# Performance work log

Hardware: AMD Instinct MI355X
Metric: run time of the kernel (lower is better)

## Reference

```python
import jax, jax.numpy as jnp
import numpy as np

ALPHA = 0.25
GAMMA = 2.0
W_CLASS = W_BBOX = W_GIOU = W_MASK = W_DICE = W_PROJ = 1.0
EPS = 1e-8


def box_cxcywh_to_xyxy(b):
    cx, cy, w, h = jnp.split(b, 4, axis=-1)
    return jnp.concatenate([cx - 0.5 * w, cy - 0.5 * h, cx + 0.5 * w, cy + 0.5 * h], axis=-1)


def dice_coef(inputs, targets):
    # inputs: logits [N, D]; targets: binary [M, D]
    s = jax.nn.sigmoid(inputs)
    num = 2.0 * jnp.einsum('nd,md->nm', s, targets)
    den = s.sum(-1)[:, None] + targets.sum(-1)[None, :]
    return (num + 1.0) / (den + 1.0)  # [N, M]


def sigmoid_focal_coef(inputs, targets):
    # inputs: logits [N, D]; targets: binary [M, D] -> [N, M]
    x = inputs[:, None, :]
    t = targets[None, :, :]
    p = jax.nn.sigmoid(x)
    # BCE-with-logits, numerically stable
    ce = jnp.maximum(x, 0.0) - x * t + jnp.log1p(jnp.exp(-jnp.abs(x)))
    p_t = p * t + (1.0 - p) * (1.0 - t)
    alpha_t = ALPHA * t + (1.0 - ALPHA) * (1.0 - t)
    return (alpha_t * ce * (1.0 - p_t) ** GAMMA).mean(-1)


def giou_cost(src_xyxy, tgt_xyxy):
    # src [nf, nq, 4], tgt [nf, 1, 4] -> cost [nf, nq, 1]
    a1 = (src_xyxy[..., 2] - src_xyxy[..., 0]) * (src_xyxy[..., 3] - src_xyxy[..., 1])
    a2 = (tgt_xyxy[..., 2] - tgt_xyxy[..., 0]) * (tgt_xyxy[..., 3] - tgt_xyxy[..., 1])
    lt = jnp.maximum(src_xyxy[:, :, None, :2], tgt_xyxy[:, None, :, :2])
    rb = jnp.minimum(src_xyxy[:, :, None, 2:], tgt_xyxy[:, None, :, 2:])
    wh = jnp.clip(rb - lt, 0.0)
    inter = wh[..., 0] * wh[..., 1]
    union = a1[:, :, None] + a2[:, None, :] - inter
    iou = inter / union
    ltc = jnp.minimum(src_xyxy[:, :, None, :2], tgt_xyxy[:, None, :, :2])
    rbc = jnp.maximum(src_xyxy[:, :, None, 2:], tgt_xyxy[:, None, :, 2:])
    whc = jnp.clip(rbc - ltc, 0.0)
    areac = whc[..., 0] * whc[..., 1]
    giou = iou - (areac - union) / areac
    return -giou


def cost_matrix_one(logits, boxes, masks, tmask, tbox, tvalid):
    # logits [nf,nq,1], boxes [nf,nq,4], masks [nf,nq,H,W], tmask [nf,H,W], tbox [nf,4], tvalid [nf]
    p = jax.nn.sigmoid(logits[..., 0])  # [nf, nq]
    neg = (1.0 - ALPHA) * p ** GAMMA * (-jnp.log(1.0 - p + EPS))
    pos = ALPHA * (1.0 - p) ** GAMMA * (-jnp.log(p + EPS))
    w = (tvalid != 0).astype(p.dtype)  # valid-frame mask replaces python `continue`
    cost_class = (((pos - neg) * w[:, None]).sum(0) / w.sum())[:, None]  # [nq, 1]

    cost_bbox = jnp.abs(boxes[:, :, None, :] - tbox[:, None, None, :]).sum(-1).mean(0)  # [nq, 1]
    cost_giou = giou_cost(box_cxcywh_to_xyxy(boxes), box_cxcywh_to_xyxy(tbox[:, None, :])).mean(0)

    out_mask = jnp.transpose(masks, (1, 0, 2, 3))  # [nq, nf, H, W]
    nq = out_mask.shape[0]
    flat_src = out_mask.reshape(nq, -1)
    flat_tgt = tmask.reshape(1, -1)
    cost_mask = sigmoid_focal_coef(flat_src, flat_tgt)  # [nq, 1]
    cost_dice = -dice_coef(flat_src, flat_tgt)

    src_y = jnp.max(out_mask, axis=2, keepdims=True).reshape(nq, -1)  # [nq, nf*W]
    src_x = jnp.max(out_mask, axis=3, keepdims=True).reshape(nq, -1)  # [nq, nf*H]
    tgt_y = jnp.max(tmask[None], axis=2, keepdims=True).reshape(1, -1)
    tgt_x = jnp.max(tmask[None], axis=3, keepdims=True).reshape(1, -1)
    cost_proj = -0.5 * (dice_coef(src_y, tgt_y) + dice_coef(src_x, tgt_x))

    C = (W_CLASS * cost_class + W_BBOX * cost_bbox + W_GIOU * cost_giou
         + W_MASK * cost_mask + W_DICE * cost_dice + W_PROJ * cost_proj)
    return C  # [nq, 1]


def setup_inputs() -> dict:
    key = jax.random.key(0)
    k = jax.random.split(key, 6)
    bs, nf, nq, H, W = 2, 8, 300, 96, 96
    pred_logits = jax.random.normal(k[0], (bs, nf, nq, 1), dtype=jnp.float32)
    pred_boxes = jax.random.uniform(k[1], (bs, nf, nq, 4), dtype=jnp.float32)
    pred_masks = jax.random.normal(k[2], (bs, nf, nq, H, W), dtype=jnp.float32)
    target_masks = (jax.random.uniform(k[3], (bs, nf, H, W)) < 0.3).astype(jnp.float32)
    tgt_boxes = jax.random.uniform(k[4], (bs, nf, 4), dtype=jnp.float32)
    tgt_valid = jnp.ones((bs, nf), dtype=jnp.int32)
    valid_pad = jnp.zeros((bs, H, W), dtype=bool)
    return {"pred_logits": pred_logits, "pred_boxes": pred_boxes, "pred_masks": pred_masks,
            "target_masks": target_masks, "tgt_boxes": tgt_boxes, "tgt_valid": tgt_valid,
            "valid_pad": valid_pad}


def reference(pred_logits, pred_boxes, pred_masks, target_masks, tgt_boxes, tgt_valid, valid_pad):
    # zero out predictions over padded regions (masked_fill with valid[:, None, None])
    masks = jnp.where(valid_pad[:, None, None, :, :], 0.0, pred_masks)
    C = jax.vmap(cost_matrix_one)(pred_logits, pred_boxes, masks, target_masks, tgt_boxes, tgt_valid)
    src_ind = jnp.argmin(C, axis=1).astype(jnp.int64)  # [bs, 1]
    tgt_ind = jnp.zeros_like(src_ind)
    return C, src_ind, tgt_ind
```

## Files before the change

### kernel.cpp

```cpp
#include <hip/hip_runtime.h>
#include <math.h>

#define NF 8
#define NQ 300
#define HSZ 96
#define WSZ 96
#define HW (HSZ*WSZ)
#define DTOT (NF*HW)
#define NT 256
#define NBF 16

#define WS_TGTY 0
#define WS_TGTX 1536
#define WS_TSUM 3072
#define WS_YSUM 3088
#define WS_XSUM 3104
#define WS_PART 4096

__device__ __forceinline__ float sigmoid_fast(float x) {
    float e = __expf(-fabsf(x));
    float inv = __builtin_amdgcn_rcpf(1.f + e);
    return x >= 0.f ? inv : e * inv;
}

__device__ __forceinline__ float blockSum(float v, float* red) {
    #pragma unroll
    for (int off = 32; off > 0; off >>= 1) v += __shfl_down(v, off, 64);
    int wid = threadIdx.x >> 6, lane = threadIdx.x & 63;
    __syncthreads();
    if (lane == 0) red[wid] = v;
    __syncthreads();
    return red[0] + red[1] + red[2] + red[3];
}

__global__ __launch_bounds__(NT)
void targets_kernel(const float* __restrict__ tm, float* __restrict__ ws) {
    int bf = blockIdx.x, t = threadIdx.x;
    __shared__ float tile[HSZ * 97];
    __shared__ float red[4];
    const float* base = tm + (size_t)bf * HW;
    float tsum = 0.f;
    #pragma unroll
    for (int it = 0; it < 36; ++it) {
        int e = it * NT + t;
        float v = base[e];
        tsum += v;
        tile[e + e / 96] = v;
    }
    __syncthreads();
    float ysum = 0.f, xsum = 0.f;
    if (t < 96) {
        float m = -INFINITY;
        #pragma unroll 8
        for (int h = 0; h < HSZ; ++h) m = fmaxf(m, tile[h * 97 + t]);
        ws[WS_TGTY + bf * 96 + t] = m;
        ysum = m;
    } else if (t < 192) {
        int hh = t - 96;
        float m = -INFINITY;
        #pragma unroll 8
        for (int w = 0; w < WSZ; ++w) m = fmaxf(m, tile[hh * 97 + w]);
        ws[WS_TGTX + bf * 96 + hh] = m;
        xsum = m;
    }
    tsum = blockSum(tsum, red);
    ysum = blockSum(ysum, red);
    xsum = blockSum(xsum, red);
    if (t == 0) {
        ws[WS_TSUM + bf] = tsum;
        ws[WS_YSUM + bf] = ysum;
        ws[WS_XSUM + bf] = xsum;
    }
}

__global__ __launch_bounds__(NT, 8)
void partial_kernel(const float* __restrict__ masks, const float* __restrict__ tmask,
                    const unsigned char* __restrict__ vpad, const float* __restrict__ ws,
                    float* __restrict__ part) {
    int bf = blockIdx.x / NQ;
    int q  = blockIdx.x - bf * NQ;
    int b  = bf >> 3;
    int t  = threadIdx.x;

    __shared__ unsigned short tile[HSZ * 98];
    __shared__ float red[4];

    const float4* mrow = (const float4*)(masks + (size_t)(bf * NQ + q) * HW);
    const float4* trow = (const float4*)(tmask + (size_t)bf * HW);
    const unsigned* prow = (const unsigned*)(vpad + (size_t)b * HW);

    float focal = 0.f, dnum = 0.f, dden = 0.f;

    #pragma unroll
    for (int it = 0; it < 9; ++it) {
        int i4 = it * NT + t;
        float4 xv = mrow[i4];
        float4 tv = trow[i4];
        unsigned pv = prow[i4];
        int h = i4 / 24;
        int c = (i4 - h * 24) * 4;

        float xs[4] = {xv.x, xv.y, xv.z, xv.w};
        float ts[4] = {tv.x, tv.y, tv.z, tv.w};
        unsigned short us[4];
        #pragma unroll
        for (int j = 0; j < 4; ++j) {
            float x = ((pv >> (8 * j)) & 0xFFu) ? 0.f : xs[j];
            float tg = ts[j];
            float ee = __expf(-fabsf(x));
            float se = 1.f + ee;
            float inv = __builtin_amdgcn_rcpf(se);
            float s = x >= 0.f ? inv : ee * inv;
            float L = __logf(se);
            float ce = fmaxf(x, 0.f) - x * tg + L;
            float omp = s + tg - 2.f * s * tg;
            float at = 0.75f - 0.5f * tg;
            focal = fmaf(at * ce, omp * omp, focal);
            dnum = fmaf(s, tg, dnum);
            dden += s;
            us[j] = (unsigned short)(__float_as_uint(x) >> 16);
        }
        int ta = h * 98 + c;
        *(unsigned*)&tile[ta]     = (unsigned)us[0] | ((unsigned)us[1] << 16);
        *(unsigned*)&tile[ta + 2] = (unsigned)us[2] | ((unsigned)us[3] << 16);
    }
    __syncthreads();

    float pYn = 0.f, pYd = 0.f, pXn = 0.f, pXd = 0.f;
    if (t < 96) {
        float m = -INFINITY;
        #pragma unroll 8
        for (int h = 0; h < HSZ; ++h)
            m = fmaxf(m, __uint_as_float((unsigned)tile[h * 98 + t] << 16));
        float sg = sigmoid_fast(m);
        pYd = sg;
        pYn = sg * ws[WS_TGTY + bf * 96 + t];
    } else if (t < 192) {
        int hh = t - 96;
        float m = -INFINITY;
        #pragma unroll 8
        for (int w = 0; w < WSZ; ++w)
            m = fmaxf(m, __uint_as_float((unsigned)tile[hh * 98 + w] << 16));
        float sg = sigmoid_fast(m);
        pXd = sg;
        pXn = sg * ws[WS_TGTX + bf * 96 + hh];
    }

    focal = blockSum(focal, red);
    dnum  = blockSum(dnum, red);
    dden  = blockSum(dden, red);
    pYn   = blockSum(pYn, red);
    pYd   = blockSum(pYd, red);
    pXn   = blockSum(pXn, red);
    pXd   = blockSum(pXd, red);

    if (t == 0) {
        float* p = part + (size_t)blockIdx.x * 8;
        p[0] = focal; p[1] = dnum; p[2] = dden;
        p[3] = pYn;   p[4] = pYd;  p[5] = pXn;  p[6] = pXd;
    }
}

__global__ __launch_bounds__(NT)
void combine_kernel(const float* __restrict__ logits, const float* __restrict__ boxes,
                    const float* __restrict__ tbox, const int* __restrict__ tvalid,
                    const float* __restrict__ ws, float* __restrict__ out) {
    int gid = blockIdx.x * NT + threadIdx.x;
    if (gid >= 2 * NQ) return;
    int b = gid / NQ, q = gid - b * NQ;

    float focal = 0.f, dnum = 0.f, dden = 0.f;
    float pYn = 0.f, pYd = 0.f, pXn = 0.f, pXd = 0.f;
    float tsum = 0.f, ysum = 0.f, xsum = 0.f;
    #pragma unroll
    for (int f = 0; f < NF; ++f) {
        int bf = b * NF + f;
        const float* p = ws + WS_PART + (size_t)(bf * NQ + q) * 8;
        focal += p[0]; dnum += p[1]; dden += p[2];
        pYn += p[3]; pYd += p[4]; pXn += p[5]; pXd += p[6];
        tsum += ws[WS_TSUM + bf];
        ysum += ws[WS_YSUM + bf];
        xsum += ws[WS_XSUM + bf];
    }
    float cost_mask = focal / (float)DTOT;
    float cost_dice = -(2.f * dnum + 1.f) / (dden + tsum + 1.f);
    float coefY = (2.f * pYn + 1.f) / (pYd + ysum + 1.f);
    float coefX = (2.f * pXn + 1.f) / (pXd + xsum + 1.f);
    float cost_proj = -0.5f * (coefY + coefX);

    float wsum = 0.f, cls = 0.f, cb = 0.f, cg = 0.f;
    #pragma unroll
    for (int f = 0; f < NF; ++f) {
        float wv = (tvalid[b * NF + f] != 0) ? 1.f : 0.f;
        wsum += wv;
        float lg = logits[(b * NF + f) * NQ + q];
        float p = sigmoid_fast(lg);
        float negc = 0.75f * p * p * (-__logf(1.f - p + 1e-8f));
        float posc = 0.25f * (1.f - p) * (1.f - p) * (-__logf(p + 1e-8f));
        cls += (posc - negc) * wv;

        const float* bx = boxes + (size_t)((b * NF + f) * NQ + q) * 4;
        const float* tb = tbox + (b * NF + f) * 4;
        float cx = bx[0], cy = bx[1], bw = bx[2], bh = bx[3];
        float tcx = tb[0], tcy = tb[1], tbw = tb[2], tbh = tb[3];
        cb += fabsf(cx - tcx) + fabsf(cy - tcy) + fabsf(bw - tbw) + fabsf(bh - tbh);
        float sx1 = cx - 0.5f * bw, sy1 = cy - 0.5f * bh;
        float sx2 = cx + 0.5f * bw, sy2 = cy + 0.5f * bh;
        float tx1 = tcx - 0.5f * tbw, ty1 = tcy - 0.5f * tbh;
        float tx2 = tcx + 0.5f * tbw, ty2 = tcy + 0.5f * tbh;
        float a1 = (sx2 - sx1) * (sy2 - sy1), a2 = (tx2 - tx1) * (ty2 - ty1);
        float iw = fmaxf(fminf(sx2, tx2) - fmaxf(sx1, tx1), 0.f);
        float ih = fmaxf(fminf(sy2, ty2) - fmaxf(sy1, ty1), 0.f);
        float inter = iw * ih;
        float uni = a1 + a2 - inter;
        float iou = inter / uni;
        float cw = fmaxf(fmaxf(sx2, tx2) - fminf(sx1, tx1), 0.f);
        float chh = fmaxf(fmaxf(sy2, ty2) - fminf(sy1, ty1), 0.f);
        float areac = cw * chh;
        cg += -(iou - (areac - uni) / areac);
    }
    cls /= wsum;
    cb *= 0.125f;
    cg *= 0.125f;
    out[b * NQ + q] = cls + cb + cg + cost_mask + cost_dice + cost_proj;
}

__global__ __launch_bounds__(NT)
void argmin_kernel(float* __restrict__ out, int write_idx) {
    int b = blockIdx.x, t = threadIdx.x;
    float best = INFINITY;
    int bi = 0x7fffffff;
    for (int q = t; q < NQ; q += NT) {
        float v = out[b * NQ + q];
        if (v < best) { best = v; bi = q; }
    }
    #pragma unroll
    for (int off = 32; off > 0; off >>= 1) {
        float ov = __shfl_down(best, off, 64);
        int oi = __shfl_down(bi, off, 64);
        if (ov < best || (ov == best && oi < bi)) { best = ov; bi = oi; }
    }
    __shared__ float rv[4];
    __shared__ int ri[4];
    int wid = t >> 6, lane = t & 63;
    if (lane == 0) { rv[wid] = best; ri[wid] = bi; }
    __syncthreads();
    if (t == 0 && write_idx) {
        #pragma unroll
        for (int w = 1; w < 4; ++w) {
            if (rv[w] < best || (rv[w] == best && ri[w] < bi)) { best = rv[w]; bi = ri[w]; }
        }
        out[2 * NQ + b] = (float)bi;
        out[2 * NQ + 2 + b] = 0.f;
    }
}

extern "C" void kernel_launch(void* const* d_in, const int* in_sizes, int n_in,
                              void* d_out, int out_size, void* d_ws, size_t ws_size,
                              hipStream_t stream) {
    const float* logits = (const float*)d_in[0];
    const float* boxes  = (const float*)d_in[1];
    const float* masks  = (const float*)d_in[2];
    const float* tmask  = (const float*)d_in[3];
    const float* tbox   = (const float*)d_in[4];
    const int*   tvalid = (const int*)d_in[5];
    const unsigned char* vpad = (const unsigned char*)d_in[6];
    float* out = (float*)d_out;
    float* ws  = (float*)d_ws;

    targets_kernel<<<NBF, NT, 0, stream>>>(tmask, ws);
    partial_kernel<<<NBF * NQ, NT, 0, stream>>>(masks, tmask, vpad, ws, ws + WS_PART);
    combine_kernel<<<(2 * NQ + NT - 1) / NT, NT, 0, stream>>>(logits, boxes, tbox,
                                                              tvalid, ws, out);
    int write_idx = (out_size >= 2 * NQ + 4) ? 1 : 0;
    argmin_kernel<<<2, NT, 0, stream>>>(out, write_idx);
}
```

Baseline: 308.8 us.

## Bit-pack target and padding masks, compute row/col maxes in registers

The targets kernel now packs the binary target mask and the padding mask into bitsets with wave ballots. The partial kernel reads a few bits per element instead of a full float target and a byte pad, which cuts the redundant per-query reloads of those arrays. The partial kernel also drops the bf16 shared tile transposes in favour of per-thread running column maxes and per-row partial maxes. It uses 192 threads, batches the seven block reductions into one pass and writes partials in the layout the combine kernel reads. The gain rests on the target tile being re-read per query, and the bitset relies on targets being exactly 0/1.

Measured after the change: 303.6 us. Within noise of the previous version (-1.7%).

```diff
diff --git a/kernel.cpp b/kernel.cpp
--- a/kernel.cpp
+++ b/kernel.cpp
@@ -7,15 +7,16 @@
 #define WSZ 96
 #define HW (HSZ*WSZ)
 #define DTOT (NF*HW)
-#define NT 256
 #define NBF 16
 
-#define WS_TGTY 0
-#define WS_TGTX 1536
-#define WS_TSUM 3072
-#define WS_YSUM 3088
-#define WS_XSUM 3104
-#define WS_PART 4096
+#define WS_TGTY  0
+#define WS_TGTX  1536
+#define WS_TSUM  3072
+#define WS_YSUM  3088
+#define WS_XSUM  3104
+#define WS_TBITS 3136
+#define WS_PBITS 7744
+#define WS_PART  8320
 
 __device__ __forceinline__ float sigmoid_fast(float x) {
     float e = __expf(-fabsf(x));
@@ -23,31 +24,43 @@
     return x >= 0.f ? inv : e * inv;
 }
 
-__device__ __forceinline__ float blockSum(float v, float* red) {
-    #pragma unroll
-    for (int off = 32; off > 0; off >>= 1) v += __shfl_down(v, off, 64);
-    int wid = threadIdx.x >> 6, lane = threadIdx.x & 63;
-    __syncthreads();
-    if (lane == 0) red[wid] = v;
-    __syncthreads();
-    return red[0] + red[1] + red[2] + red[3];
-}
-
-__global__ __launch_bounds__(NT)
-void targets_kernel(const float* __restrict__ tm, float* __restrict__ ws) {
+#define NTT 1024
+__global__ __launch_bounds__(NTT)
+void targets_kernel(const float* __restrict__ tm, const unsigned char* __restrict__ vpad,
+                    float* __restrict__ ws) {
     int bf = blockIdx.x, t = threadIdx.x;
+    int lane = t & 63, wid = t >> 6;
     __shared__ float tile[HSZ * 97];
-    __shared__ float red[4];
+    __shared__ float redt[16 * 3];
     const float* base = tm + (size_t)bf * HW;
+    unsigned* tbw = (unsigned*)(ws + WS_TBITS) + bf * 288;
+
     float tsum = 0.f;
     #pragma unroll
-    for (int it = 0; it < 36; ++it) {
-        int e = it * NT + t;
+    for (int it = 0; it < 9; ++it) {
+        int e = it * NTT + t;
         float v = base[e];
         tsum += v;
         tile[e + e / 96] = v;
-    }
-    __syncthreads();
+        unsigned long long m = __ballot(v != 0.f);
+        int word = it * 32 + wid * 2;
+        if (lane == 0)       tbw[word]     = (unsigned)m;
+        else if (lane == 32) tbw[word + 1] = (unsigned)(m >> 32);
+    }
+    if ((bf & 7) == 0) {
+        const unsigned char* vb = vpad + (size_t)(bf >> 3) * HW;
+        unsigned* pbw = (unsigned*)(ws + WS_PBITS) + (bf >> 3) * 288;
+        #pragma unroll
+        for (int it = 0; it < 9; ++it) {
+            int e = it * NTT + t;
+            unsigned long long m = __ballot(vb[e] != 0);
+            int word = it * 32 + wid * 2;
+            if (lane == 0)       pbw[word]     = (unsigned)m;
+            else if (lane == 32) pbw[word + 1] = (unsigned)(m >> 32);
+        }
+    }
+    __syncthreads();
+
     float ysum = 0.f, xsum = 0.f;
     if (t < 96) {
         float m = -INFINITY;
@@ -63,119 +76,147 @@
         ws[WS_TGTX + bf * 96 + hh] = m;
         xsum = m;
     }
-    tsum = blockSum(tsum, red);
-    ysum = blockSum(ysum, red);
-    xsum = blockSum(xsum, red);
+    float s0 = tsum, s1 = ysum, s2 = xsum;
+    #pragma unroll
+    for (int off = 32; off > 0; off >>= 1) {
+        s0 += __shfl_down(s0, off, 64);
+        s1 += __shfl_down(s1, off, 64);
+        s2 += __shfl_down(s2, off, 64);
+    }
+    if (lane == 0) { redt[wid * 3] = s0; redt[wid * 3 + 1] = s1; redt[wid * 3 + 2] = s2; }
+    __syncthreads();
     if (t == 0) {
-        ws[WS_TSUM + bf] = tsum;
-        ws[WS_YSUM + bf] = ysum;
-        ws[WS_XSUM + bf] = xsum;
-    }
-}
-
-__global__ __launch_bounds__(NT, 8)
-void partial_kernel(const float* __restrict__ masks, const float* __restrict__ tmask,
-                    const unsigned char* __restrict__ vpad, const float* __restrict__ ws,
+        float a0 = 0.f, a1 = 0.f, a2 = 0.f;
+        #pragma unroll
+        for (int w = 0; w < 16; ++w) {
+            a0 += redt[w * 3]; a1 += redt[w * 3 + 1]; a2 += redt[w * 3 + 2];
+        }
+        ws[WS_TSUM + bf] = a0;
+        ws[WS_YSUM + bf] = a1;
+        ws[WS_XSUM + bf] = a2;
+    }
+}
+
+#define NTP 192
+__global__ __launch_bounds__(NTP, 4)
+void partial_kernel(const float* __restrict__ masks, const float* __restrict__ ws,
                     float* __restrict__ part) {
-    int bf = blockIdx.x / NQ;
-    int q  = blockIdx.x - bf * NQ;
-    int b  = bf >> 3;
+    int bid = blockIdx.x;
+    int bf = bid / NQ;
+    int q  = bid - bf * NQ;
+    int b  = bf >> 3, f = bf & 7;
     int t  = threadIdx.x;
-
-    __shared__ unsigned short tile[HSZ * 98];
-    __shared__ float red[4];
-
-    const float4* mrow = (const float4*)(masks + (size_t)(bf * NQ + q) * HW);
-    const float4* trow = (const float4*)(tmask + (size_t)bf * HW);
-    const unsigned* prow = (const unsigned*)(vpad + (size_t)b * HW);
+    int w4 = t % 24;
+    int r0 = t / 24;
+    int wsh = (t & 7) * 4;
+
+    __shared__ float rp[96 * 25];
+    __shared__ float cp[8 * 100];
+    __shared__ float red[3][8];
+
+    const float4* mrow = (const float4*)(masks + (size_t)bid * HW);
+    const unsigned* tbw = (const unsigned*)(ws + WS_TBITS) + bf * 288;
+    const unsigned* pbw = (const unsigned*)(ws + WS_PBITS) + b * 288;
 
     float focal = 0.f, dnum = 0.f, dden = 0.f;
-
-    #pragma unroll
-    for (int it = 0; it < 9; ++it) {
-        int i4 = it * NT + t;
+    float cm0 = -INFINITY, cm1 = -INFINITY, cm2 = -INFINITY, cm3 = -INFINITY;
+
+    #pragma unroll
+    for (int k = 0; k < 12; ++k) {
+        int i4 = k * NTP + t;
         float4 xv = mrow[i4];
-        float4 tv = trow[i4];
-        unsigned pv = prow[i4];
-        int h = i4 / 24;
-        int c = (i4 - h * 24) * 4;
-
+        unsigned tn = (tbw[k * 24 + (t >> 3)] >> wsh) & 0xFu;
+        unsigned pn = (pbw[k * 24 + (t >> 3)] >> wsh) & 0xFu;
         float xs[4] = {xv.x, xv.y, xv.z, xv.w};
-        float ts[4] = {tv.x, tv.y, tv.z, tv.w};
-        unsigned short us[4];
+        if (pn) {
+            #pragma unroll
+            for (int j = 0; j < 4; ++j) if ((pn >> j) & 1u) xs[j] = 0.f;
+        }
+        float rmx = -INFINITY;
         #pragma unroll
         for (int j = 0; j < 4; ++j) {
-            float x = ((pv >> (8 * j)) & 0xFFu) ? 0.f : xs[j];
-            float tg = ts[j];
-            float ee = __expf(-fabsf(x));
-            float se = 1.f + ee;
+            float x = xs[j];
+            float tg = (float)((tn >> j) & 1u);
+            float e = __expf(-fabsf(x));
+            float se = 1.f + e;
             float inv = __builtin_amdgcn_rcpf(se);
-            float s = x >= 0.f ? inv : ee * inv;
+            float s = x >= 0.f ? inv : e * inv;
             float L = __logf(se);
-            float ce = fmaxf(x, 0.f) - x * tg + L;
-            float omp = s + tg - 2.f * s * tg;
-            float at = 0.75f - 0.5f * tg;
+            float ce = fmaf(-x, tg, fmaxf(x, 0.f) + L);
+            float omp = fmaf(tg, fmaf(-2.f, s, 1.f), s);
+            float at = fmaf(tg, -0.5f, 0.75f);
             focal = fmaf(at * ce, omp * omp, focal);
             dnum = fmaf(s, tg, dnum);
             dden += s;
-            us[j] = (unsigned short)(__float_as_uint(x) >> 16);
-        }
-        int ta = h * 98 + c;
-        *(unsigned*)&tile[ta]     = (unsigned)us[0] | ((unsigned)us[1] << 16);
-        *(unsigned*)&tile[ta + 2] = (unsigned)us[2] | ((unsigned)us[3] << 16);
-    }
-    __syncthreads();
-
-    float pYn = 0.f, pYd = 0.f, pXn = 0.f, pXd = 0.f;
+            rmx = fmaxf(rmx, x);
+        }
+        cm0 = fmaxf(cm0, xs[0]); cm1 = fmaxf(cm1, xs[1]);
+        cm2 = fmaxf(cm2, xs[2]); cm3 = fmaxf(cm3, xs[3]);
+        rp[(8 * k + r0) * 25 + w4] = rmx;
+    }
+    {
+        float4 cmv = {cm0, cm1, cm2, cm3};
+        *(float4*)&cp[r0 * 100 + w4 * 4] = cmv;
+    }
+    __syncthreads();
+
+    float v0 = focal, v1 = dnum, v2 = dden, v3 = 0.f, v4 = 0.f, v5 = 0.f, v6 = 0.f;
     if (t < 96) {
-        float m = -INFINITY;
-        #pragma unroll 8
-        for (int h = 0; h < HSZ; ++h)
-            m = fmaxf(m, __uint_as_float((unsigned)tile[h * 98 + t] << 16));
+        float m = cp[t];
+        #pragma unroll
+        for (int p = 1; p < 8; ++p) m = fmaxf(m, cp[p * 100 + t]);
         float sg = sigmoid_fast(m);
-        pYd = sg;
-        pYn = sg * ws[WS_TGTY + bf * 96 + t];
-    } else if (t < 192) {
-        int hh = t - 96;
-        float m = -INFINITY;
-        #pragma unroll 8
-        for (int w = 0; w < WSZ; ++w)
-            m = fmaxf(m, __uint_as_float((unsigned)tile[hh * 98 + w] << 16));
+        v4 = sg;
+        v3 = sg * ws[WS_TGTY + bf * 96 + t];
+    } else {
+        int r = t - 96;
+        float m = rp[r * 25];
+        #pragma unroll
+        for (int c = 1; c < 24; ++c) m = fmaxf(m, rp[r * 25 + c]);
         float sg = sigmoid_fast(m);
-        pXd = sg;
-        pXn = sg * ws[WS_TGTX + bf * 96 + hh];
-    }
-
-    focal = blockSum(focal, red);
-    dnum  = blockSum(dnum, red);
-    dden  = blockSum(dden, red);
-    pYn   = blockSum(pYn, red);
-    pYd   = blockSum(pYd, red);
-    pXn   = blockSum(pXn, red);
-    pXd   = blockSum(pXd, red);
-
+        v6 = sg;
+        v5 = sg * ws[WS_TGTX + bf * 96 + r];
+    }
+    #pragma unroll
+    for (int off = 32; off > 0; off >>= 1) {
+        v0 += __shfl_down(v0, off, 64);
+        v1 += __shfl_down(v1, off, 64);
+        v2 += __shfl_down(v2, off, 64);
+        v3 += __shfl_down(v3, off, 64);
+        v4 += __shfl_down(v4, off, 64);
+        v5 += __shfl_down(v5, off, 64);
+        v6 += __shfl_down(v6, off, 64);
+    }
+    int wid = t >> 6, lane = t & 63;
+    if (lane == 0) {
+        red[wid][0] = v0; red[wid][1] = v1; red[wid][2] = v2; red[wid][3] = v3;
+        red[wid][4] = v4; red[wid][5] = v5; red[wid][6] = v6;
+    }
+    __syncthreads();
     if (t == 0) {
-        float* p = part + (size_t)blockIdx.x * 8;
-        p[0] = focal; p[1] = dnum; p[2] = dden;
-        p[3] = pYn;   p[4] = pYd;  p[5] = pXn;  p[6] = pXd;
-    }
-}
-
-__global__ __launch_bounds__(NT)
+        float* o = part + (size_t)((b * NQ + q) * NF + f) * 8;
+        #pragma unroll
+        for (int i = 0; i < 7; ++i) o[i] = red[0][i] + red[1][i] + red[2][i];
+    }
+}
+
+#define NTC 64
+__global__ __launch_bounds__(NTC)
 void combine_kernel(const float* __restrict__ logits, const float* __restrict__ boxes,
                     const float* __restrict__ tbox, const int* __restrict__ tvalid,
                     const float* __restrict__ ws, float* __restrict__ out) {
-    int gid = blockIdx.x * NT + threadIdx.x;
+    int gid = blockIdx.x * NTC + threadIdx.x;
     if (gid >= 2 * NQ) return;
     int b = gid / NQ, q = gid - b * NQ;
 
+    const float* pbase = ws + WS_PART + (size_t)gid * (NF * 8);
     float focal = 0.f, dnum = 0.f, dden = 0.f;
     float pYn = 0.f, pYd = 0.f, pXn = 0.f, pXd = 0.f;
     float tsum = 0.f, ysum = 0.f, xsum = 0.f;
     #pragma unroll
     for (int f = 0; f < NF; ++f) {
         int bf = b * NF + f;
-        const float* p = ws + WS_PART + (size_t)(bf * NQ + q) * 8;
+        const float* p = pbase + f * 8;
         focal += p[0]; dnum += p[1]; dden += p[2];
         pYn += p[3]; pYd += p[4]; pXn += p[5]; pXd += p[6];
         tsum += ws[WS_TSUM + bf];
@@ -225,6 +266,7 @@
     out[b * NQ + q] = cls + cb + cg + cost_mask + cost_dice + cost_proj;
 }
 
+#define NT 256
 __global__ __launch_bounds__(NT)
 void argmin_kernel(float* __restrict__ out, int write_idx) {
     int b = blockIdx.x, t = threadIdx.x;
@@ -268,10 +310,10 @@
     float* out = (float*)d_out;
     float* ws  = (float*)d_ws;
 
-    targets_kernel<<<NBF, NT, 0, stream>>>(tmask, ws);
-    partial_kernel<<<NBF * NQ, NT, 0, stream>>>(masks, tmask, vpad, ws, ws + WS_PART);
-    combine_kernel<<<(2 * NQ + NT - 1) / NT, NT, 0, stream>>>(logits, boxes, tbox,
-                                                              tvalid, ws, out);
+    targets_kernel<<<NBF, NTT, 0, stream>>>(tmask, vpad, ws);
+    partial_kernel<<<NBF * NQ, NTP, 0, stream>>>(masks, ws, ws + WS_PART);
+    combine_kernel<<<(2 * NQ + NTC - 1) / NTC, NTC, 0, stream>>>(logits, boxes, tbox,
+                                                                 tvalid, ws, out);
     int write_idx = (out_size >= 2 * NQ + 4) ? 1 : 0;
     argmin_kernel<<<2, NT, 0, stream>>>(out, write_idx);
 }
```
